# Performance work log

Hardware: AMD Instinct MI355X
Metric: run time of the kernel (lower is better)

Reference implementation:

```python
import jax, jax.numpy as jnp
import numpy as np

S, D, H, F = 4096, 2048, 16, 8192
HD = D // H
EPS = 1e-5


def setup_inputs() -> dict:
    key = jax.random.key(0)
    ks = jax.random.split(key, 16)
    sc_d = 1.0 / np.sqrt(D)
    sc_f = 1.0 / np.sqrt(F)
    return {
        "x": jax.random.normal(ks[0], (S, D), dtype=jnp.float32),
        # stacked per-head projections: [H, D, HD]
        "Wq": jax.random.normal(ks[1], (H, D, HD), dtype=jnp.float32) * sc_d,
        "bq": jax.random.normal(ks[2], (H, HD), dtype=jnp.float32) * 0.01,
        "Wk": jax.random.normal(ks[3], (H, D, HD), dtype=jnp.float32) * sc_d,
        "bk": jax.random.normal(ks[4], (H, HD), dtype=jnp.float32) * 0.01,
        "Wv": jax.random.normal(ks[5], (H, D, HD), dtype=jnp.float32) * sc_d,
        "bv": jax.random.normal(ks[6], (H, HD), dtype=jnp.float32) * 0.01,
        "Wp": jax.random.normal(ks[7], (D, D), dtype=jnp.float32) * sc_d,
        "bp": jax.random.normal(ks[8], (D,), dtype=jnp.float32) * 0.01,
        "W1": jax.random.normal(ks[9], (D, F), dtype=jnp.float32) * sc_d,
        "b1": jax.random.normal(ks[10], (F,), dtype=jnp.float32) * 0.01,
        "W2": jax.random.normal(ks[11], (F, D), dtype=jnp.float32) * sc_f,
        "b2": jax.random.normal(ks[12], (D,), dtype=jnp.float32) * 0.01,
        "gamma": jnp.ones((D,), dtype=jnp.float32),
        "beta": jnp.zeros((D,), dtype=jnp.float32),
    }


def _layernorm(x, gamma, beta):
    mu = jnp.mean(x, axis=-1, keepdims=True)
    var = jnp.var(x, axis=-1, keepdims=True)
    return (x - mu) * jax.lax.rsqrt(var + EPS) * gamma + beta


def reference(x, Wq, bq, Wk, bk, Wv, bv, Wp, bp, W1, b1, W2, b2, gamma, beta):
    residual = x
    # batched per-head projections: [H, S, HD]
    q = jnp.einsum('sd,hde->hse', x, Wq) + bq[:, None, :]
    k = jnp.einsum('sd,hde->hse', x, Wk) + bk[:, None, :]
    v = jnp.einsum('sd,hde->hse', x, Wv) + bv[:, None, :]
    scores = jnp.einsum('hse,hte->hst', q, k) / np.sqrt(HD).astype(np.float32)
    attn = jax.nn.softmax(scores, axis=-1)
    heads = jnp.einsum('hst,hte->hse', attn, v)  # [H, S, HD]
    # concat heads along feature dim (head 0 first): [S, H*HD]
    heads = jnp.transpose(heads, (1, 0, 2)).reshape(S, H * HD)
    out = heads @ Wp + bp
    # residual_attn=True, norm_attn=True
    out = out + residual
    out = _layernorm(out, gamma, beta)
    # feedforward (original forward ends here)
    out = jax.nn.relu(out @ W1 + b1) @ W2 + b2
    return out
```

## Files before the change

### kernel.cpp

```cpp
#include <hip/hip_runtime.h>
#include <hip/hip_bf16.h>
#include <cstdint>
#include <cstddef>

#define S 4096
#define D 2048
#define H 16
#define HD 128
#define F 8192

typedef unsigned short ushort_t;
typedef __attribute__((ext_vector_type(8))) short short8;
typedef __attribute__((ext_vector_type(4))) float floatx4;

__device__ __forceinline__ ushort_t f2bf(float f) {
  union { float f; unsigned u; } v; v.f = f;
  unsigned u = v.u;
  return (ushort_t)((u + 0x7fffu + ((u >> 16) & 1u)) >> 16);
}

__device__ __forceinline__ void async16(void* lds, const void* g) {
  __builtin_amdgcn_global_load_lds(
      (const __attribute__((address_space(1))) unsigned int*)g,
      (__attribute__((address_space(3))) unsigned int*)lds, 16, 0, 0);
}

template <int N>
__device__ __forceinline__ void vmcnt_() {
  static_assert(N >= 0 && N <= 8, "vmcnt range");
  if constexpr (N == 0) asm volatile("s_waitcnt vmcnt(0)" ::: "memory");
  else if constexpr (N == 1) asm volatile("s_waitcnt vmcnt(1)" ::: "memory");
  else if constexpr (N == 2) asm volatile("s_waitcnt vmcnt(2)" ::: "memory");
  else if constexpr (N == 3) asm volatile("s_waitcnt vmcnt(3)" ::: "memory");
  else if constexpr (N == 4) asm volatile("s_waitcnt vmcnt(4)" ::: "memory");
  else if constexpr (N == 5) asm volatile("s_waitcnt vmcnt(5)" ::: "memory");
  else if constexpr (N == 6) asm volatile("s_waitcnt vmcnt(6)" ::: "memory");
  else if constexpr (N == 7) asm volatile("s_waitcnt vmcnt(7)" ::: "memory");
  else asm volatile("s_waitcnt vmcnt(8)" ::: "memory");
}
__device__ __forceinline__ void bar_() { asm volatile("s_barrier" ::: "memory"); }
__device__ __forceinline__ void lgkm0_() {
  asm volatile("s_waitcnt lgkmcnt(0)" ::: "memory");
  __builtin_amdgcn_sched_barrier(0);
}


__global__ void cast_bf16(const float* __restrict__ src, ushort_t* __restrict__ dst, int n4) {
  int i = blockIdx.x * blockDim.x + threadIdx.x;
  if (i < n4) {
    float4 v = ((const float4*)src)[i];
    ushort4 o;
    o.x = f2bf(v.x); o.y = f2bf(v.y); o.z = f2bf(v.z); o.w = f2bf(v.w);
    ((ushort4*)dst)[i] = o;
  }
}

__global__ void build_bqkv(const float* __restrict__ bq, const float* __restrict__ bk,
                           const float* __restrict__ bv, float* __restrict__ bqkv) {
  int n = blockIdx.x * blockDim.x + threadIdx.x;
  if (n < 3 * D) {
    float v;
    if (n < D) v = bq[n];
    else if (n < 2 * D) v = bk[n - D];
    else v = bv[n - 2 * D];
    bqkv[n] = v;
  }
}

__global__ void transpose_f32_bf16(const float* __restrict__ src, ushort_t* __restrict__ dst,
                                   int ldS, int ldD, long srcBatchStride, long dstBatchRows) {
  __shared__ float t[32][33];
  int b = blockIdx.z;
  src += (size_t)b * srcBatchStride;
  dst += (size_t)b * dstBatchRows * ldD;
  int r0 = blockIdx.x * 32, c0 = blockIdx.y * 32;
  int tx = threadIdx.x, ty = threadIdx.y;
#pragma unroll
  for (int i = 0; i < 4; ++i)
    t[ty + i * 8][tx] = src[(size_t)(r0 + ty + i * 8) * ldS + c0 + tx];
  __syncthreads();
#pragma unroll
  for (int i = 0; i < 4; ++i)
    dst[(size_t)(c0 + ty + i * 8) * ldD + r0 + tx] = f2bf(t[tx][ty + i * 8]);
}

__global__ void transpose_bf16(const ushort_t* __restrict__ src, ushort_t* __restrict__ dst,
                               int ldS, int ldD, int colOff) {
  __shared__ ushort_t t[32][33];
  int r0 = blockIdx.x * 32, c0 = blockIdx.y * 32;
  int tx = threadIdx.x, ty = threadIdx.y;
#pragma unroll
  for (int i = 0; i < 4; ++i)
    t[ty + i * 8][tx] = src[(size_t)(r0 + ty + i * 8) * ldS + colOff + c0 + tx];
  __syncthreads();
#pragma unroll
  for (int i = 0; i < 4; ++i)
    dst[(size_t)(c0 + ty + i * 8) * ldD + r0 + tx] = t[tx][ty + i * 8];
}

template <int MODE, int BM>
__global__ __launch_bounds__(512, 2)
void gemm8p(const ushort_t* __restrict__ A, const ushort_t* __restrict__ Bt,
            const float* __restrict__ bias, const float* __restrict__ resid,
            ushort_t* __restrict__ outb, float* __restrict__ outf,
            int M, int N, int K, int gridN) {
  constexpr int MQ = BM / 64;
  constexpr int LA = BM / 128;
  __shared__ __align__(16) ushort_t Abuf[2][BM * 64];
  __shared__ __align__(16) ushort_t Bbuf[2][256 * 64];

  const int tid = threadIdx.x;
  const int l = tid & 63, w = tid >> 6;
  const int c16 = l & 15, g = l >> 4;
  const int wm = w >> 2, wn = w & 3;

  const int nwg = gridDim.x;
  const int q8 = nwg >> 3, r8 = nwg & 7;
  const int xcd = blockIdx.x & 7, bix = blockIdx.x >> 3;
  const int wgid = (xcd < r8 ? xcd * (q8 + 1) : r8 * (q8 + 1) + (xcd - r8) * q8) + bix;
  const int m0 = (wgid / gridN) * BM;
  const int n0 = (wgid % gridN) * 256;

  const size_t Kb = (size_t)K * 2;
  const size_t aHalfB = (size_t)(BM / 2) * Kb;
  const size_t bHalfB = (size_t)128 * Kb;

  const char* aSrc[LA]; char* aLds[LA];
#pragma unroll
  for (int i = 0; i < LA; ++i) {
    int ch = i * 512 + tid;
    int row = ch >> 3;
    aSrc[i] = (const char*)A + (size_t)(m0 + row) * Kb + (((ch ^ row) & 7) << 4);
    aLds[i] = (char*)(&Abuf[0][0]) + ch * 16;
  }
  const char* bSrc[2]; char* bLds[2];
#pragma unroll
  for (int i = 0; i < 2; ++i) {
    int ch = i * 512 + tid;
    int row = ch >> 3;
    bSrc[i] = (const char*)Bt + (size_t)(n0 + row) * Kb + (((ch ^ row) & 7) << 4);
    bLds[i] = (char*)(&Bbuf[0][0]) + ch * 16;
  }

  auto stA = [&](int p, int h, int kByte) {
#pragma unroll
    for (int i = 0; i < LA; ++i)
      async16(aLds[i] + p * (BM * 128) + h * (BM * 64), aSrc[i] + (size_t)h * aHalfB + kByte);
  };
  auto stB = [&](int p, int h, int kByte) {
#pragma unroll
    for (int i = 0; i < 2; ++i)
      async16(bLds[i] + p * 32768 + h * 16384, bSrc[i] + (size_t)h * bHalfB + kByte);
  };

  int rdK[2];
  rdK[0] = ((g ^ (c16 & 7)) << 4);
  rdK[1] = (((4 + g) ^ (c16 & 7)) << 4);
  const char* Ab0 = (const char*)(&Abuf[0][0]);
  const char* Ab1 = Ab0 + BM * 128;
  const char* Bb0 = (const char*)(&Bbuf[0][0]);
  const char* Bb1 = Bb0 + 32768;

  floatx4 acc[2][2][MQ][2];
#pragma unroll
  for (int ah = 0; ah < 2; ++ah)
#pragma unroll
    for (int bh = 0; bh < 2; ++bh)
#pragma unroll
      for (int mf = 0; mf < MQ; ++mf)
#pragma unroll
        for (int nf = 0; nf < 2; ++nf) acc[ah][bh][mf][nf] = (floatx4){0.f, 0.f, 0.f, 0.f};

  short8 af[MQ][2], bf0[2][2], bf1[2][2];
  auto ldA = [&](const char* base, int h) {
#pragma unroll
    for (int mf = 0; mf < MQ; ++mf)
#pragma unroll
      for (int kk = 0; kk < 2; ++kk)
        af[mf][kk] = *(const short8*)(base + h * (BM * 64) +
            (wm * (BM / 4) + mf * 16 + c16) * 128 + rdK[kk]);
  };
  auto ldB = [&](const char* base, int h, short8 (&bf)[2][2]) {
#pragma unroll
    for (int nf = 0; nf < 2; ++nf)
#pragma unroll
      for (int kk = 0; kk < 2; ++kk)
        bf[nf][kk] = *(const short8*)(base + h * 16384 +
            (wn * 32 + nf * 16 + c16) * 128 + rdK[kk]);
  };
  auto mma2 = [&](int ah) {
    __builtin_amdgcn_s_setprio(1);
#pragma unroll
    for (int mf = 0; mf < MQ; ++mf)
#pragma unroll
      for (int kk = 0; kk < 2; ++kk) {
#pragma unroll
        for (int nf = 0; nf < 2; ++nf)
          acc[ah][0][mf][nf] = __builtin_amdgcn_mfma_f32_16x16x32_bf16(
              af[mf][kk], bf0[nf][kk], acc[ah][0][mf][nf], 0, 0, 0);
#pragma unroll
        for (int nf = 0; nf < 2; ++nf)
          acc[ah][1][mf][nf] = __builtin_amdgcn_mfma_f32_16x16x32_bf16(
              af[mf][kk], bf1[nf][kk], acc[ah][1][mf][nf], 0, 0, 0);
      }
    __builtin_amdgcn_s_setprio(0);
  };

  stA(0, 0, 0); stB(0, 0, 0); stB(0, 1, 0); stA(0, 1, 0);
  stA(1, 0, 128); stB(1, 0, 128); stB(1, 1, 128);
  vmcnt_<LA + 4>();
  bar_();

  const int NI = K >> 7;
  for (int i = 0; i < NI; ++i) {
    const bool lastI = (i == NI - 1);
    const int kE = i << 8;

    ldA(Ab0, 0); ldB(Bb0, 0, bf0); ldB(Bb0, 1, bf1);
    stA(1, 1, kE + 128);
    bar_(); lgkm0_();
    mma2(0);
    bar_();

    ldA(Ab0, 1);
    if (!lastI) { stA(0, 0, kE + 256); stB(0, 0, kE + 256); stB(0, 1, kE + 256); }
    bar_(); lgkm0_();
    mma2(1);
    if (lastI) vmcnt_<0>(); else vmcnt_<LA + 4>();
    bar_();

    ldA(Ab1, 0); ldB(Bb1, 0, bf0); ldB(Bb1, 1, bf1);
    if (!lastI) stA(0, 1, kE + 256);
    bar_(); lgkm0_();
    mma2(0);
    bar_();

    ldA(Ab1, 1);
    if (!lastI) { stA(1, 0, kE + 384); stB(1, 0, kE + 384); stB(1, 1, kE + 384); }
    bar_(); lgkm0_();
    mma2(1);
    if (!lastI) { vmcnt_<LA + 4>(); bar_(); }
  }

#pragma unroll
  for (int ah = 0; ah < 2; ++ah)
#pragma unroll
    for (int bh = 0; bh < 2; ++bh)
#pragma unroll
      for (int nf = 0; nf < 2; ++nf) {
        int gcol = n0 + bh * 128 + wn * 32 + nf * 16 + c16;
        float bj = bias[gcol];
#pragma unroll
        for (int mf = 0; mf < MQ; ++mf) {
          int grow = m0 + ah * (BM / 2) + wm * (BM / 4) + mf * 16 + g * 4;
#pragma unroll
          for (int r = 0; r < 4; ++r) {
            float v = acc[ah][bh][mf][nf][r] + bj;
            size_t o = (size_t)(grow + r) * N + gcol;
            if (MODE == 0) {
              outb[o] = f2bf(v);
            } else if (MODE == 1) {
              outf[o] = v + resid[o];
            } else if (MODE == 2) {
              outb[o] = f2bf(v > 0.f ? v : 0.f);
            } else {
              outf[o] = v;
            }
          }
        }
      }
}

__global__ __launch_bounds__(256, 2)
void attn_kernel(const ushort_t* __restrict__ QKV, const ushort_t* __restrict__ Vt,
                 ushort_t* __restrict__ heads) {
  const int h = blockIdx.y;
  const int tid = threadIdx.x, w = tid >> 6, l = tid & 63;
  const int g = l >> 4, c = l & 15;
  const int q0 = blockIdx.x * 128 + w * 32;
  const float scale = 0.08838834764831845f;

  __shared__ __align__(16) ushort_t Ks[2][64 * 128];
  __shared__ __align__(16) ushort_t Vs[128 * 64];
  __shared__ __align__(16) ushort_t Ps[4][2][16][72];

  short8 qf[2][4];
#pragma unroll
  for (int u = 0; u < 2; ++u)
#pragma unroll
    for (int k0 = 0; k0 < 4; ++k0)
      qf[u][k0] = *(const short8*)(QKV + (size_t)(q0 + u * 16 + c) * (3 * D) + h * HD + k0 * 32 + g * 8);

  floatx4 o[2][8];
#pragma unroll
  for (int u = 0; u < 2; ++u)
#pragma unroll
    for (int j = 0; j < 8; ++j) o[u][j] = (floatx4){0.f, 0.f, 0.f, 0.f};
  float l_run[2] = {0.f, 0.f};

#pragma unroll
  for (int cc = 0; cc < 4; ++cc) {
    int slot = cc * 256 + tid;
    int krow = slot >> 4, kch = slot & 15;
    const char* gk = (const char*)QKV +
        ((size_t)krow * (3 * D) + D + h * HD) * 2 + ((kch ^ (krow & 15)) << 4);
    async16((char*)(&Ks[0][0]) + (size_t)(cc * 256 + w * 64) * 16, gk);
  }

  for (int t0 = 0, ti = 0; t0 < S; t0 += 64, ++ti) {
    const int cur = ti & 1, nxt = cur ^ 1;
    const bool lastT = (t0 + 64 >= S);

#pragma unroll
    for (int cc = 0; cc < 4; ++cc) {
      int slot = cc * 256 + tid;
      int vrow = slot >> 3, vch = slot & 7;
      const char* gv = (const char*)Vt +
          ((size_t)(h * HD + vrow) * S + t0) * 2 + ((vch ^ (vrow & 7)) << 4);
      async16((char*)Vs + (size_t)(cc * 256 + w * 64) * 16, gv);
    }
    if (!lastT) {
#pragma unroll
      for (int cc = 0; cc < 4; ++cc) {
        int slot = cc * 256 + tid;
        int krow = slot >> 4, kch = slot & 15;
        const char* gk = (const char*)QKV +
            ((size_t)(t0 + 64 + krow) * (3 * D) + D + h * HD) * 2 + ((kch ^ (krow & 15)) << 4);
        async16((char*)(&Ks[0][0]) + (size_t)(nxt * 1024 + cc * 256 + w * 64) * 16, gk);
      }
    }
    if (lastT) vmcnt_<4>(); else vmcnt_<8>();
    bar_();

    const ushort_t* Kb = &Ks[cur][0];
    floatx4 sc[2][4];
#pragma unroll
    for (int u = 0; u < 2; ++u)
#pragma unroll
      for (int tt = 0; tt < 4; ++tt) sc[u][tt] = (floatx4){0.f, 0.f, 0.f, 0.f};
#pragma unroll
    for (int tt = 0; tt < 4; ++tt) {
      short8 kf[4];
#pragma unroll
      for (int k0 = 0; k0 < 4; ++k0)
        kf[k0] = *(const short8*)(Kb + (tt * 16 + c) * 128 + (((k0 * 4 + g) ^ c) << 3));
#pragma unroll
      for (int u = 0; u < 2; ++u)
#pragma unroll
        for (int k0 = 0; k0 < 4; ++k0)
          sc[u][tt] = __builtin_amdgcn_mfma_f32_16x16x32_bf16(kf[k0], qf[u][k0], sc[u][tt], 0, 0, 0);
    }

#pragma unroll
    for (int u = 0; u < 2; ++u) {
#pragma unroll
      for (int tt = 0; tt < 4; ++tt) {
        float p0 = __expf(sc[u][tt][0] * scale);
        float p1 = __expf(sc[u][tt][1] * scale);
        float p2 = __expf(sc[u][tt][2] * scale);
        float p3 = __expf(sc[u][tt][3] * scale);
        l_run[u] += p0 + p1 + p2 + p3;
        unsigned r0, r1;
        asm("v_cvt_pk_bf16_f32 %0, %1, %2" : "=v"(r0) : "v"(p0), "v"(p1));
        asm("v_cvt_pk_bf16_f32 %0, %1, %2" : "=v"(r1) : "v"(p2), "v"(p3));
        uint2 pk; pk.x = r0; pk.y = r1;
        *reinterpret_cast<uint2*>(&Ps[w][u][c][tt * 16 + g * 4]) = pk;
      }
    }
    __asm__ volatile("s_waitcnt lgkmcnt(0)" ::: "memory");
    if (lastT) vmcnt_<0>(); else vmcnt_<4>();
    bar_();

    short8 pf[2][2];
#pragma unroll
    for (int u = 0; u < 2; ++u)
#pragma unroll
      for (int tk = 0; tk < 2; ++tk)
        pf[u][tk] = *reinterpret_cast<const short8*>(&Ps[w][u][c][tk * 32 + g * 8]);
#pragma unroll
    for (int j = 0; j < 8; ++j) {
#pragma unroll
      for (int tk = 0; tk < 2; ++tk) {
        short8 vf = *(const short8*)(Vs + (j * 16 + c) * 64 + (((tk * 4 + g) ^ (c & 7)) << 3));
#pragma unroll
        for (int u = 0; u < 2; ++u)
          o[u][j] = __builtin_amdgcn_mfma_f32_16x16x32_bf16(pf[u][tk], vf, o[u][j], 0, 0, 0);
      }
    }
    bar_();
  }

#pragma unroll
  for (int u = 0; u < 2; ++u) {
    float lt = l_run[u];
    lt += __shfl_xor(lt, 16);
    lt += __shfl_xor(lt, 32);
    float linv[4];
#pragma unroll
    for (int r = 0; r < 4; ++r) linv[r] = 1.f / __shfl(lt, g * 4 + r);
    ushort_t* hp = heads + (size_t)(q0 + u * 16 + g * 4) * D + h * HD + c;
#pragma unroll
    for (int j = 0; j < 8; ++j)
#pragma unroll
      for (int r = 0; r < 4; ++r)
        hp[(size_t)r * D + j * 16] = f2bf(o[u][j][r] * linv[r]);
  }
}

__global__ __launch_bounds__(256)
void ln_kernel(const float* __restrict__ preln, const float* __restrict__ gamma,
               const float* __restrict__ beta, ushort_t* __restrict__ y) {
  int row = blockIdx.x, tid = threadIdx.x;
  const float* p = preln + (size_t)row * D;
  float vals[8];
  float sum = 0.f, ss = 0.f;
#pragma unroll
  for (int k = 0; k < 8; ++k) {
    float v = p[tid + k * 256];
    vals[k] = v; sum += v; ss += v * v;
  }
#pragma unroll
  for (int off = 32; off >= 1; off >>= 1) {
    sum += __shfl_xor(sum, off);
    ss += __shfl_xor(ss, off);
  }
  __shared__ float s1[4], s2[4];
  int w = tid >> 6, l = tid & 63;
  if (l == 0) { s1[w] = sum; s2[w] = ss; }
  __syncthreads();
  sum = s1[0] + s1[1] + s1[2] + s1[3];
  ss = s2[0] + s2[1] + s2[2] + s2[3];
  float mu = sum / (float)D;
  float var = ss / (float)D - mu * mu;
  float rs = rsqrtf(var + 1e-5f);
  ushort_t* yr = y + (size_t)row * D;
#pragma unroll
  for (int k = 0; k < 8; ++k) {
    int d = tid + k * 256;
    yr[d] = f2bf((vals[k] - mu) * rs * gamma[d] + beta[d]);
  }
}


extern "C" void kernel_launch(void* const* d_in, const int* in_sizes, int n_in,
                              void* d_out, int out_size, void* d_ws, size_t ws_size,
                              hipStream_t stream) {
  const float* x = (const float*)d_in[0];
  const float* Wq = (const float*)d_in[1];
  const float* bq = (const float*)d_in[2];
  const float* Wk = (const float*)d_in[3];
  const float* bk = (const float*)d_in[4];
  const float* Wv = (const float*)d_in[5];
  const float* bv = (const float*)d_in[6];
  const float* Wp = (const float*)d_in[7];
  const float* bp = (const float*)d_in[8];
  const float* W1 = (const float*)d_in[9];
  const float* b1 = (const float*)d_in[10];
  const float* W2 = (const float*)d_in[11];
  const float* b2 = (const float*)d_in[12];
  const float* gamma = (const float*)d_in[13];
  const float* beta = (const float*)d_in[14];

  char* ws = (char*)d_ws;
  ushort_t* WQKVT = (ushort_t*)(ws + 0);
  ushort_t* XB    = (ushort_t*)(ws + 25165824);
  float*    BQKV  = (float*)(ws + 41943040);
  ushort_t* WPT   = (ushort_t*)(ws + 41975808);
  ushort_t* W1T   = (ushort_t*)(ws + 50364416);
  ushort_t* W2T   = (ushort_t*)(ws + 83918848);
  ushort_t* QKV   = (ushort_t*)(ws + 117473280);
  ushort_t* HEADS = (ushort_t*)(ws + 167804928);
  ushort_t* VT    = (ushort_t*)(ws + 184582144);
  float*    PRELN = (float*)(ws + 0);
  ushort_t* AB    = (ushort_t*)(ws + 117473280);
  ushort_t* Y     = (ushort_t*)(ws + 184582144);
  float* OUT = (float*)d_out;

  dim3 tb(32, 8);
  cast_bf16<<<(S * D / 4 + 255) / 256, 256, 0, stream>>>(x, XB, S * D / 4);
  build_bqkv<<<(3 * D + 255) / 256, 256, 0, stream>>>(bq, bk, bv, BQKV);
  transpose_f32_bf16<<<dim3(D / 32, HD / 32, H), tb, 0, stream>>>(Wq, WQKVT, HD, D, (long)D * HD, HD);
  transpose_f32_bf16<<<dim3(D / 32, HD / 32, H), tb, 0, stream>>>(Wk, WQKVT + (size_t)D * D, HD, D, (long)D * HD, HD);
  transpose_f32_bf16<<<dim3(D / 32, HD / 32, H), tb, 0, stream>>>(Wv, WQKVT + (size_t)2 * D * D, HD, D, (long)D * HD, HD);
  transpose_f32_bf16<<<dim3(D / 32, D / 32, 1), tb, 0, stream>>>(Wp, WPT, D, D, 0, 0);
  transpose_f32_bf16<<<dim3(D / 32, F / 32, 1), tb, 0, stream>>>(W1, W1T, F, D, 0, 0);
  transpose_f32_bf16<<<dim3(F / 32, D / 32, 1), tb, 0, stream>>>(W2, W2T, D, F, 0, 0);
  gemm8p<0, 128><<<dim3((S / 128) * (3 * D / 256)), 512, 0, stream>>>(
      XB, WQKVT, BQKV, nullptr, QKV, nullptr, S, 3 * D, D, 3 * D / 256);
  transpose_bf16<<<dim3(S / 32, D / 32), tb, 0, stream>>>(QKV, VT, 3 * D, S, 2 * D);
  attn_kernel<<<dim3(S / 128, H), 256, 0, stream>>>(QKV, VT, HEADS);
  gemm8p<1, 128><<<dim3((S / 128) * (D / 256)), 512, 0, stream>>>(
      HEADS, WPT, bp, x, nullptr, PRELN, S, D, D, D / 256);
  ln_kernel<<<S, 256, 0, stream>>>(PRELN, gamma, beta, Y);
  gemm8p<2, 256><<<dim3((S / 256) * (F / 256)), 512, 0, stream>>>(
      Y, W1T, b1, nullptr, AB, nullptr, S, F, D, F / 256);
  gemm8p<3, 128><<<dim3((S / 128) * (D / 256)), 512, 0, stream>>>(
      AB, W2T, b2, nullptr, nullptr, OUT, S, D, F, D / 256);
}
```

Measured before the change: 926.8 us.

## Double-buffer V tiles and interleave softmax with PV in attention

The attention kernel now double-buffers V in LDS alongside K, so the next K and V tiles are prefetched together. This removes the mid-iteration barrier that used to wait for V. V fragments are loaded into registers up front, and softmax for the second query sub-tile is interleaved with the PV MFMAs of the first, using a single per-warp P scratch buffer. The QKV projection GEMM also switches to a 256-row tile, which raises register pressure and LDS use and may reduce occupancy.

After: 903.0 us. 2.6% less time.

```diff
diff --git a/kernel.cpp b/kernel.cpp
--- a/kernel.cpp
+++ b/kernel.cpp
@@ -281,8 +281,8 @@
   const float scale = 0.08838834764831845f;
 
   __shared__ __align__(16) ushort_t Ks[2][64 * 128];
-  __shared__ __align__(16) ushort_t Vs[128 * 64];
-  __shared__ __align__(16) ushort_t Ps[4][2][16][72];
+  __shared__ __align__(16) ushort_t Vs[2][128 * 64];
+  __shared__ __align__(16) ushort_t Ps[4][16][72];
 
   short8 qf[2][4];
 #pragma unroll
@@ -298,41 +298,48 @@
     for (int j = 0; j < 8; ++j) o[u][j] = (floatx4){0.f, 0.f, 0.f, 0.f};
   float l_run[2] = {0.f, 0.f};
 
-#pragma unroll
-  for (int cc = 0; cc < 4; ++cc) {
-    int slot = cc * 256 + tid;
-    int krow = slot >> 4, kch = slot & 15;
-    const char* gk = (const char*)QKV +
-        ((size_t)krow * (3 * D) + D + h * HD) * 2 + ((kch ^ (krow & 15)) << 4);
-    async16((char*)(&Ks[0][0]) + (size_t)(cc * 256 + w * 64) * 16, gk);
-  }
-
-  for (int t0 = 0, ti = 0; t0 < S; t0 += 64, ++ti) {
-    const int cur = ti & 1, nxt = cur ^ 1;
-    const bool lastT = (t0 + 64 >= S);
-
+  auto stageK = [&](int buf, int t0) {
+#pragma unroll
+    for (int cc = 0; cc < 4; ++cc) {
+      int slot = cc * 256 + tid;
+      int krow = slot >> 4, kch = slot & 15;
+      const char* gk = (const char*)QKV +
+          ((size_t)(t0 + krow) * (3 * D) + D + h * HD) * 2 + ((kch ^ (krow & 15)) << 4);
+      async16((char*)(&Ks[0][0]) + (size_t)(buf * 1024 + cc * 256 + w * 64) * 16, gk);
+    }
+  };
+  auto stageV = [&](int buf, int t0) {
 #pragma unroll
     for (int cc = 0; cc < 4; ++cc) {
       int slot = cc * 256 + tid;
       int vrow = slot >> 3, vch = slot & 7;
       const char* gv = (const char*)Vt +
           ((size_t)(h * HD + vrow) * S + t0) * 2 + ((vch ^ (vrow & 7)) << 4);
-      async16((char*)Vs + (size_t)(cc * 256 + w * 64) * 16, gv);
+      async16((char*)(&Vs[0][0]) + (size_t)(buf * 1024 + cc * 256 + w * 64) * 16, gv);
     }
-    if (!lastT) {
-#pragma unroll
-      for (int cc = 0; cc < 4; ++cc) {
-        int slot = cc * 256 + tid;
-        int krow = slot >> 4, kch = slot & 15;
-        const char* gk = (const char*)QKV +
-            ((size_t)(t0 + 64 + krow) * (3 * D) + D + h * HD) * 2 + ((kch ^ (krow & 15)) << 4);
-        async16((char*)(&Ks[0][0]) + (size_t)(nxt * 1024 + cc * 256 + w * 64) * 16, gk);
-      }
-    }
-    if (lastT) vmcnt_<4>(); else vmcnt_<8>();
+  };
+
+  stageK(0, 0);
+  stageV(0, 0);
+
+  for (int t0 = 0, ti = 0; t0 < S; t0 += 64, ++ti) {
+    const int cur = ti & 1, nxt = cur ^ 1;
+    const bool lastT = (t0 + 64 >= S);
+
+    if (!lastT) { stageK(nxt, t0 + 64); stageV(nxt, t0 + 64); }
+    if (lastT) vmcnt_<0>(); else vmcnt_<8>();
     bar_();
 
     const ushort_t* Kb = &Ks[cur][0];
+    const ushort_t* Vb = &Vs[cur][0];
+
+    short8 vf[8][2];
+#pragma unroll
+    for (int j = 0; j < 8; ++j)
+#pragma unroll
+      for (int tk = 0; tk < 2; ++tk)
+        vf[j][tk] = *(const short8*)(Vb + (j * 16 + c) * 64 + (((tk * 4 + g) ^ (c & 7)) << 3));
+
     floatx4 sc[2][4];
 #pragma unroll
     for (int u = 0; u < 2; ++u)
@@ -351,8 +358,7 @@
           sc[u][tt] = __builtin_amdgcn_mfma_f32_16x16x32_bf16(kf[k0], qf[u][k0], sc[u][tt], 0, 0, 0);
     }
 
-#pragma unroll
-    for (int u = 0; u < 2; ++u) {
+    auto smax = [&](int u) {
 #pragma unroll
       for (int tt = 0; tt < 4; ++tt) {
         float p0 = __expf(sc[u][tt][0] * scale);
@@ -364,29 +370,33 @@
         asm("v_cvt_pk_bf16_f32 %0, %1, %2" : "=v"(r0) : "v"(p0), "v"(p1));
         asm("v_cvt_pk_bf16_f32 %0, %1, %2" : "=v"(r1) : "v"(p2), "v"(p3));
         uint2 pk; pk.x = r0; pk.y = r1;
-        *reinterpret_cast<uint2*>(&Ps[w][u][c][tt * 16 + g * 4]) = pk;
+        *reinterpret_cast<uint2*>(&Ps[w][c][tt * 16 + g * 4]) = pk;
       }
-    }
-    __asm__ volatile("s_waitcnt lgkmcnt(0)" ::: "memory");
-    if (lastT) vmcnt_<0>(); else vmcnt_<4>();
-    bar_();
-
-    short8 pf[2][2];
-#pragma unroll
-    for (int u = 0; u < 2; ++u)
-#pragma unroll
-      for (int tk = 0; tk < 2; ++tk)
-        pf[u][tk] = *reinterpret_cast<const short8*>(&Ps[w][u][c][tk * 32 + g * 8]);
-#pragma unroll
-    for (int j = 0; j < 8; ++j) {
-#pragma unroll
-      for (int tk = 0; tk < 2; ++tk) {
-        short8 vf = *(const short8*)(Vs + (j * 16 + c) * 64 + (((tk * 4 + g) ^ (c & 7)) << 3));
-#pragma unroll
-        for (int u = 0; u < 2; ++u)
-          o[u][j] = __builtin_amdgcn_mfma_f32_16x16x32_bf16(pf[u][tk], vf, o[u][j], 0, 0, 0);
-      }
-    }
+    };
+    auto pv = [&](int u, short8 (&pf)[2]) {
+#pragma unroll
+      for (int j = 0; j < 8; ++j)
+#pragma unroll
+        for (int tk = 0; tk < 2; ++tk)
+          o[u][j] = __builtin_amdgcn_mfma_f32_16x16x32_bf16(pf[tk], vf[j][tk], o[u][j], 0, 0, 0);
+    };
+
+    short8 pf0[2], pf1[2];
+    smax(0);
+    lgkm0_();
+#pragma unroll
+    for (int tk = 0; tk < 2; ++tk)
+      pf0[tk] = *reinterpret_cast<const short8*>(&Ps[w][c][tk * 32 + g * 8]);
+    lgkm0_();
+    smax(1);
+    pv(0, pf0);
+    lgkm0_();
+#pragma unroll
+    for (int tk = 0; tk < 2; ++tk)
+      pf1[tk] = *reinterpret_cast<const short8*>(&Ps[w][c][tk * 32 + g * 8]);
+    lgkm0_();
+    pv(1, pf1);
+
     bar_();
   }
 
@@ -485,7 +495,7 @@
   transpose_f32_bf16<<<dim3(D / 32, D / 32, 1), tb, 0, stream>>>(Wp, WPT, D, D, 0, 0);
   transpose_f32_bf16<<<dim3(D / 32, F / 32, 1), tb, 0, stream>>>(W1, W1T, F, D, 0, 0);
   transpose_f32_bf16<<<dim3(F / 32, D / 32, 1), tb, 0, stream>>>(W2, W2T, D, F, 0, 0);
-  gemm8p<0, 128><<<dim3((S / 128) * (3 * D / 256)), 512, 0, stream>>>(
+  gemm8p<0, 256><<<dim3((S / 256) * (3 * D / 256)), 512, 0, stream>>>(
       XB, WQKVT, BQKV, nullptr, QKV, nullptr, S, 3 * D, D, 3 * D / 256);
   transpose_bf16<<<dim3(S / 32, D / 32), tb, 0, stream>>>(QKV, VT, 3 * D, S, 2 * D);
   attn_kernel<<<dim3(S / 128, H), 256, 0, stream>>>(QKV, VT, HEADS);
```
